# Performance work log

Hardware: AMD Instinct MI355X
Metric: run time of the kernel (lower is better)

The kernel has to match this reference:

```python
import jax, jax.numpy as jnp
import numpy as np

B, T, I, H, O = 128, 512, 512, 2048, 512  # batch, seq_length, input, hidden, output


def setup_inputs() -> dict:
    key = jax.random.key(0)
    ks = jax.random.split(key, 8)
    s_ih = 1.0 / np.sqrt(H)  # torch RNNCell/Linear default init scale 1/sqrt(hidden)
    body = jax.random.normal(ks[0], (B, T - 1, I), dtype=jnp.float32)
    # last timestep row stores the integer pad index (as float), per the module's protocol
    pad = jax.random.randint(ks[1], (B,), 0, T - 2)
    last = jnp.broadcast_to(pad[:, None, None].astype(jnp.float32), (B, 1, I))
    x = jnp.concatenate([body, last], axis=1)  # [B, T, I]
    W_ih = jax.random.uniform(ks[2], (H, I), jnp.float32, -s_ih, s_ih)
    W_hh = jax.random.uniform(ks[3], (H, H), jnp.float32, -s_ih, s_ih)
    b_ih = jax.random.uniform(ks[4], (H,), jnp.float32, -s_ih, s_ih)
    b_hh = jax.random.uniform(ks[5], (H,), jnp.float32, -s_ih, s_ih)
    W_fc = jax.random.uniform(ks[6], (O, H), jnp.float32, -s_ih, s_ih)
    b_fc = jax.random.uniform(ks[7], (O,), jnp.float32, -s_ih, s_ih)
    h0 = jnp.ones((H,), jnp.float32)  # self.h parameter, ones-initialized
    return {"x": x, "h0": h0, "W_ih": W_ih, "b_ih": b_ih, "W_hh": W_hh,
            "b_hh": b_hh, "W_fc": W_fc, "b_fc": b_fc}


def reference(x, h0, W_ih, b_ih, W_hh, b_hh, W_fc, b_fc):
    steps = T - 2  # loop runs over x.shape[2]-1 = (T-1)-1 timesteps
    pad = x[:, -1, 0].astype(jnp.int32)          # [B] pad indices
    xs = jnp.transpose(x[:, :steps, :], (1, 0, 2))  # [steps, B, I]
    h_init = jnp.broadcast_to(h0, (x.shape[0], H))  # self.h * ones([B,1])

    def step(h, xt):
        h = jnp.tanh(xt @ W_ih.T + b_ih + h @ W_hh.T + b_hh)
        return h, h @ W_fc.T + b_fc

    _, outs = jax.lax.scan(step, h_init, xs)     # [steps, B, O]
    # mask selects the single timestep j == pad_len[b]; everything else is zeroed
    mask = (pad[None, :] == jnp.arange(steps)[:, None]).astype(outs.dtype)  # [steps, B]
    return jnp.sum(outs * mask[:, :, None], axis=0)  # [B, O]
```

## Files before the change

kernel.cpp:

```cpp
#include <hip/hip_runtime.h>

#define Bsz 128
#define Tsz 512
#define Isz 512
#define Hsz 2048
#define Osz 512
#define STEPS 510

typedef short short8 __attribute__((ext_vector_type(8)));
typedef float floatx4 __attribute__((ext_vector_type(4)));

__device__ __forceinline__ unsigned short f2bf(float f) {
  unsigned int u = __builtin_bit_cast(unsigned int, f);
  u += 0x7FFFu + ((u >> 16) & 1u);
  return (unsigned short)(u >> 16);
}

__device__ __forceinline__ float tanh_fast(float x) {
  const float e = __expf(2.f * x);
  return 1.f - 2.f * __builtin_amdgcn_rcpf(e + 1.f);
}

template <int AUX>
__device__ __forceinline__ void gload_lds16(const void* g, void* l) {
  __builtin_amdgcn_global_load_lds(
      (const __attribute__((address_space(1))) void*)g,
      (__attribute__((address_space(3))) void*)l, 16, 0, AUX);
}

__global__ __launch_bounds__(256, 1)
void rnn_kernel(const float* __restrict__ x, const float* __restrict__ h0v,
                const float* __restrict__ W_ih, const float* __restrict__ b_ih,
                const float* __restrict__ W_hh, const float* __restrict__ b_hh,
                unsigned short* __restrict__ hbuf,
                float* __restrict__ hfinal,
                unsigned int* __restrict__ flags,
                unsigned int* __restrict__ xcc_arr)
{
  __shared__ short h_lds[4 * 8192];
  __shared__ float red_lds[4 * 1024];
  __shared__ int pad_lds[16];
  __shared__ unsigned int mode_lds;

  const int tid = threadIdx.x;
  const int lane = tid & 63;
  const int wv = tid >> 6;
  const int m16 = lane & 15;
  const int quad = lane >> 4;
  const int m7 = m16 & 7;
  const int rg = blockIdx.x & 7;
  const int cg = blockIdx.x >> 3;
  const int b0 = rg * 16;
  const int c0 = cg * 64;
  const int kq = wv * 512;
  const int kqx = wv * 128;
  const int wvoff = wv * 8192;

  {
    unsigned int xcc;
    asm volatile("s_getreg_b32 %0, hwreg(HW_REG_XCC_ID)" : "=s"(xcc));
    if (tid == 0)
      __hip_atomic_store(&xcc_arr[rg * 32 + cg], xcc + 1u, __ATOMIC_RELAXED,
                         __HIP_MEMORY_SCOPE_AGENT);
    if (wv == 0) {
      const unsigned int* ap = &xcc_arr[rg * 32 + (lane & 31)];
      unsigned int v;
      do {
        v = __hip_atomic_load(ap, __ATOMIC_RELAXED, __HIP_MEMORY_SCOPE_AGENT);
        if (__all((int)(v != 0u))) break;
        __builtin_amdgcn_s_sleep(2);
      } while (true);
      const int same = __all((int)(v == xcc + 1u));
      if (tid == 0) mode_lds = (unsigned int)same;
    }
  }

  short8 wf[16][4];
  short8 wih[4][4];
#pragma unroll
  for (int nt = 0; nt < 4; ++nt) {
    const int wrow = c0 + nt * 16 + m16;
    const float* base = W_hh + (size_t)wrow * Hsz + kq + quad * 8;
#pragma unroll
    for (int kc = 0; kc < 16; ++kc) {
      short8 v;
#pragma unroll
      for (int j = 0; j < 8; ++j) v[j] = (short)f2bf(base[kc * 32 + j]);
      wf[kc][nt] = v;
    }
    const float* basex = W_ih + (size_t)wrow * Isz + kqx + quad * 8;
#pragma unroll
    for (int kc = 0; kc < 4; ++kc) {
      short8 v;
#pragma unroll
      for (int j = 0; j < 8; ++j) v[j] = (short)f2bf(basex[kc * 32 + j]);
      wih[kc][nt] = v;
    }
  }

  const int rrow = tid >> 4;
  const int rcb = (tid & 15) * 4;
  float bias[4];
#pragma unroll
  for (int i = 0; i < 4; ++i) bias[i] = b_ih[c0 + rcb + i] + b_hh[c0 + rcb + i];

  if (tid < 16)
    pad_lds[tid] = (int)x[(size_t)(b0 + tid) * (Tsz * Isz) + (size_t)(Tsz - 1) * Isz];

  for (int i = lane; i < 1024; i += 64) {
    const int c = i >> 7;
    const int r = (i >> 3) & 15;
    const int u = i & 7;
    const int k = kq + c * 64 + u * 8;
    short8 v;
#pragma unroll
    for (int j = 0; j < 8; ++j) v[j] = (short)f2bf(h0v[k + j]);
    *reinterpret_cast<short8*>(&h_lds[wvoff + c * 1024 + r * 64 + (u ^ (r & 7)) * 8]) = v;
  }

  __syncthreads();
  const bool use_l2 = (mode_lds != 0u);

  const unsigned int* fp = flags + (size_t)(wv * 8 + (lane & 7)) * 8 + rg;

  for (int t = 0; t < STEPS; ++t) {
    const bool have_next = (t + 1) < STEPS;

    const float* xp = x + (size_t)(b0 + m16) * (Tsz * Isz) + (size_t)t * Isz + kqx + quad * 8;
    float4 xv[8];
#pragma unroll
    for (int kcc = 0; kcc < 4; ++kcc) {
      xv[2 * kcc] = *reinterpret_cast<const float4*>(xp + kcc * 32);
      xv[2 * kcc + 1] = *reinterpret_cast<const float4*>(xp + kcc * 32 + 4);
    }

    if (t > 0) {
      while (!__all((int)(__hip_atomic_load(fp, __ATOMIC_RELAXED,
                                            __HIP_MEMORY_SCOPE_AGENT) >= (unsigned)t)))
        __builtin_amdgcn_s_sleep(1);
      const unsigned short* hsrcp = hbuf + (size_t)(t & 1) * (Bsz * Hsz);
      if (use_l2) {
#pragma unroll
        for (int c = 0; c < 8; ++c) {
          const unsigned short* src = hsrcp + (size_t)((wv * 8 + c) * 8 + rg) * 1024;
          gload_lds16<0x01>(src + lane * 8, &h_lds[wvoff + c * 1024]);
          gload_lds16<0x01>(src + 512 + lane * 8, &h_lds[wvoff + c * 1024 + 512]);
        }
      } else {
#pragma unroll
        for (int c = 0; c < 8; ++c) {
          const unsigned short* src = hsrcp + (size_t)((wv * 8 + c) * 8 + rg) * 1024;
          gload_lds16<0x11>(src + lane * 8, &h_lds[wvoff + c * 1024]);
          gload_lds16<0x11>(src + 512 + lane * 8, &h_lds[wvoff + c * 1024 + 512]);
        }
      }
    }

    short8 xa[4];
#pragma unroll
    for (int kcc = 0; kcc < 4; ++kcc) {
      short8 a;
      a[0] = (short)f2bf(xv[2 * kcc].x);
      a[1] = (short)f2bf(xv[2 * kcc].y);
      a[2] = (short)f2bf(xv[2 * kcc].z);
      a[3] = (short)f2bf(xv[2 * kcc].w);
      a[4] = (short)f2bf(xv[2 * kcc + 1].x);
      a[5] = (short)f2bf(xv[2 * kcc + 1].y);
      a[6] = (short)f2bf(xv[2 * kcc + 1].z);
      a[7] = (short)f2bf(xv[2 * kcc + 1].w);
      xa[kcc] = a;
    }

    floatx4 acc[4];
#pragma unroll
    for (int nt = 0; nt < 4; ++nt) {
      floatx4 zero = {0.f, 0.f, 0.f, 0.f};
      acc[nt] = zero;
    }
#pragma unroll
    for (int kcc = 0; kcc < 4; ++kcc)
#pragma unroll
      for (int nt = 0; nt < 4; ++nt)
        acc[nt] = __builtin_amdgcn_mfma_f32_16x16x32_bf16(xa[kcc], wih[kcc][nt], acc[nt], 0, 0, 0);

    __builtin_amdgcn_s_waitcnt(0x0F78);
#pragma unroll
    for (int c = 0; c < 4; ++c) {
      const int base = wvoff + c * 1024 + m16 * 64;
#pragma unroll
      for (int k2 = 0; k2 < 2; ++k2) {
        const short8 a =
            *reinterpret_cast<const short8*>(&h_lds[base + ((k2 * 4 + quad) ^ m7) * 8]);
#pragma unroll
        for (int nt = 0; nt < 4; ++nt)
          acc[nt] = __builtin_amdgcn_mfma_f32_16x16x32_bf16(a, wf[c * 2 + k2][nt], acc[nt], 0, 0, 0);
      }
    }
    __builtin_amdgcn_s_waitcnt(0x0F70);
#pragma unroll
    for (int c = 4; c < 8; ++c) {
      const int base = wvoff + c * 1024 + m16 * 64;
#pragma unroll
      for (int k2 = 0; k2 < 2; ++k2) {
        const short8 a =
            *reinterpret_cast<const short8*>(&h_lds[base + ((k2 * 4 + quad) ^ m7) * 8]);
#pragma unroll
        for (int nt = 0; nt < 4; ++nt)
          acc[nt] = __builtin_amdgcn_mfma_f32_16x16x32_bf16(a, wf[c * 2 + k2][nt], acc[nt], 0, 0, 0);
      }
    }

#pragma unroll
    for (int nt = 0; nt < 4; ++nt)
#pragma unroll
      for (int i = 0; i < 4; ++i)
        red_lds[wv * 1024 + (quad * 4 + i) * 64 + nt * 16 + m16] = acc[nt][i];

    __syncthreads();

    {
      float4 z = {0.f, 0.f, 0.f, 0.f};
#pragma unroll
      for (int ww = 0; ww < 4; ++ww) {
        const float4 p =
            *reinterpret_cast<const float4*>(&red_lds[ww * 1024 + rrow * 64 + rcb]);
        z.x += p.x; z.y += p.y; z.z += p.z; z.w += p.w;
      }
      const float t0 = tanh_fast(z.x + bias[0]);
      const float t1 = tanh_fast(z.y + bias[1]);
      const float t2 = tanh_fast(z.z + bias[2]);
      const float t3 = tanh_fast(z.w + bias[3]);
      unsigned long long pk = (unsigned long long)f2bf(t0) |
                              ((unsigned long long)f2bf(t1) << 16) |
                              ((unsigned long long)f2bf(t2) << 32) |
                              ((unsigned long long)f2bf(t3) << 48);
      const int toff = rrow * 64 + ((rcb >> 3) ^ (rrow & 7)) * 8 + ((rcb >> 2) & 1) * 4;
      unsigned short* hd = hbuf + (size_t)((t + 1) & 1) * (Bsz * Hsz) +
                           (size_t)(cg * 8 + rg) * 1024 + toff;
      if (use_l2) {
        *reinterpret_cast<unsigned long long*>(hd) = pk;
      } else {
        __hip_atomic_store(reinterpret_cast<unsigned long long*>(hd), pk,
                           __ATOMIC_RELAXED, __HIP_MEMORY_SCOPE_AGENT);
      }
      if (pad_lds[rrow] == t) {
        float4 o;
        o.x = t0; o.y = t1; o.z = t2; o.w = t3;
        *reinterpret_cast<float4*>(&hfinal[(size_t)(b0 + rrow) * Hsz + c0 + rcb]) = o;
      }
    }

    __syncthreads();

    if (have_next && tid == 0) {
      __hip_atomic_store(flags + cg * 8 + rg, (unsigned)(t + 1),
                         __ATOMIC_RELAXED, __HIP_MEMORY_SCOPE_AGENT);
    }
  }
}

__global__ __launch_bounds__(64)
void fc_kernel(const float* __restrict__ hfinal, const float* __restrict__ W_fc,
               const float* __restrict__ b_fc, float* __restrict__ out) {
  const int lane = threadIdx.x & 63;
  const int m16 = lane & 15;
  const int quad = lane >> 4;
  const int b0 = (blockIdx.x & 7) * 16;
  const int o0 = (blockIdx.x >> 3) * 16;
  floatx4 acc = {0.f, 0.f, 0.f, 0.f};
  const float* ap = hfinal + (size_t)(b0 + m16) * Hsz + quad * 8;
  const float* bp = W_fc + (size_t)(o0 + m16) * Hsz + quad * 8;
#pragma unroll 4
  for (int kc = 0; kc < 64; ++kc) {
    short8 a, b;
#pragma unroll
    for (int j = 0; j < 8; ++j) a[j] = (short)f2bf(ap[kc * 32 + j]);
#pragma unroll
    for (int j = 0; j < 8; ++j) b[j] = (short)f2bf(bp[kc * 32 + j]);
    acc = __builtin_amdgcn_mfma_f32_16x16x32_bf16(a, b, acc, 0, 0, 0);
  }
  const float bias = b_fc[o0 + m16];
#pragma unroll
  for (int i = 0; i < 4; ++i)
    out[(size_t)(b0 + quad * 4 + i) * Osz + o0 + m16] = acc[i] + bias;
}

__global__ void zero_flags(unsigned int* f) { f[blockIdx.x * 256 + threadIdx.x] = 0u; }

extern "C" void kernel_launch(void* const* d_in, const int* in_sizes, int n_in,
                              void* d_out, int out_size, void* d_ws, size_t ws_size,
                              hipStream_t stream) {
  const float* x = (const float*)d_in[0];
  const float* h0 = (const float*)d_in[1];
  const float* W_ih = (const float*)d_in[2];
  const float* b_ih = (const float*)d_in[3];
  const float* W_hh = (const float*)d_in[4];
  const float* b_hh = (const float*)d_in[5];
  const float* W_fc = (const float*)d_in[6];
  const float* b_fc = (const float*)d_in[7];
  float* out = (float*)d_out;

  char* ws = (char*)d_ws;
  unsigned short* hbuf = (unsigned short*)ws;
  float* hfinal = (float*)(ws + (1u << 20));
  unsigned int* flags = (unsigned int*)(ws + (2u << 20));
  unsigned int* xcc_arr = flags + 256;

  zero_flags<<<2, 256, 0, stream>>>(flags);
  rnn_kernel<<<256, 256, 0, stream>>>(x, h0, W_ih, b_ih, W_hh, b_hh, hbuf, hfinal,
                                      flags, xcc_arr);
  fc_kernel<<<256, 64, 0, stream>>>(hfinal, W_fc, b_fc, out);
}
```

Measured before the change: 2.070 ms.

## Prefetch next timestep's x into double-buffered LDS via async global-to-LDS loads

Replaces the per-step direct global loads of the x slice with an asynchronous global_load_lds prefetch of the next timestep into a swizzled, double-buffered LDS area, issued right after the h exchange loads. The x fetch latency can then overlap with the cross-block flag wait and the MFMA work instead of sitting at the start of each step. The vmcnt waits are re-encoded so the h halves are consumed while the x prefetch stays in flight, and __syncthreads is replaced with a barrier that only waits on lgkmcnt. The cost is extra LDS use and correctness that relies on the atomic spin or the barrier draining the prefetch before the next step reads it.

```diff
diff --git a/kernel.cpp b/kernel.cpp
--- a/kernel.cpp
+++ b/kernel.cpp
@@ -26,6 +26,10 @@
   __builtin_amdgcn_global_load_lds(
       (const __attribute__((address_space(1))) void*)g,
       (__attribute__((address_space(3))) void*)l, 16, 0, AUX);
+}
+
+__device__ __forceinline__ void barrier_lds() {
+  asm volatile("s_waitcnt lgkmcnt(0)\n\ts_barrier" ::: "memory");
 }
 
 __global__ __launch_bounds__(256, 1)
@@ -38,6 +42,7 @@
                 unsigned int* __restrict__ xcc_arr)
 {
   __shared__ short h_lds[4 * 8192];
+  __shared__ float x_lds[2 * 4 * 2048];
   __shared__ float red_lds[4 * 1024];
   __shared__ int pad_lds[16];
   __shared__ unsigned int mode_lds;
@@ -118,6 +123,16 @@
     *reinterpret_cast<short8*>(&h_lds[wvoff + c * 1024 + r * 64 + (u ^ (r & 7)) * 8]) = v;
   }
 
+  {
+#pragma unroll
+    for (int c = 0; c < 8; ++c) {
+      const int r = 2 * c + (lane >> 5);
+      const float* g = x + (size_t)(b0 + r) * (Tsz * Isz) + kqx +
+                       (((lane & 31) ^ (r & 7)) << 2);
+      gload_lds16<0>(g, &x_lds[wv * 2048 + c * 256]);
+    }
+  }
+
   __syncthreads();
   const bool use_l2 = (mode_lds != 0u);
 
@@ -125,14 +140,7 @@
 
   for (int t = 0; t < STEPS; ++t) {
     const bool have_next = (t + 1) < STEPS;
-
-    const float* xp = x + (size_t)(b0 + m16) * (Tsz * Isz) + (size_t)t * Isz + kqx + quad * 8;
-    float4 xv[8];
-#pragma unroll
-    for (int kcc = 0; kcc < 4; ++kcc) {
-      xv[2 * kcc] = *reinterpret_cast<const float4*>(xp + kcc * 32);
-      xv[2 * kcc + 1] = *reinterpret_cast<const float4*>(xp + kcc * 32 + 4);
-    }
+    const int par = t & 1;
 
     if (t > 0) {
       while (!__all((int)(__hip_atomic_load(fp, __ATOMIC_RELAXED,
@@ -156,19 +164,32 @@
       }
     }
 
+    if (have_next) {
+      const int npar = par ^ 1;
+#pragma unroll
+      for (int c = 0; c < 8; ++c) {
+        const int r = 2 * c + (lane >> 5);
+        const float* g = x + (size_t)(b0 + r) * (Tsz * Isz) + (size_t)(t + 1) * Isz +
+                         kqx + (((lane & 31) ^ (r & 7)) << 2);
+        gload_lds16<0>(g, &x_lds[(npar * 4 + wv) * 2048 + c * 256]);
+      }
+    }
+
     short8 xa[4];
-#pragma unroll
-    for (int kcc = 0; kcc < 4; ++kcc) {
-      short8 a;
-      a[0] = (short)f2bf(xv[2 * kcc].x);
-      a[1] = (short)f2bf(xv[2 * kcc].y);
-      a[2] = (short)f2bf(xv[2 * kcc].z);
-      a[3] = (short)f2bf(xv[2 * kcc].w);
-      a[4] = (short)f2bf(xv[2 * kcc + 1].x);
-      a[5] = (short)f2bf(xv[2 * kcc + 1].y);
-      a[6] = (short)f2bf(xv[2 * kcc + 1].z);
-      a[7] = (short)f2bf(xv[2 * kcc + 1].w);
-      xa[kcc] = a;
+    {
+      const float* xb = &x_lds[(par * 4 + wv) * 2048 + m16 * 128];
+#pragma unroll
+      for (int kc = 0; kc < 4; ++kc) {
+        const int u0 = kc * 8 + quad * 2;
+        const float4 a0 = *reinterpret_cast<const float4*>(&xb[(u0 ^ m7) << 2]);
+        const float4 a1 = *reinterpret_cast<const float4*>(&xb[((u0 + 1) ^ m7) << 2]);
+        short8 a;
+        a[0] = (short)f2bf(a0.x); a[1] = (short)f2bf(a0.y);
+        a[2] = (short)f2bf(a0.z); a[3] = (short)f2bf(a0.w);
+        a[4] = (short)f2bf(a1.x); a[5] = (short)f2bf(a1.y);
+        a[6] = (short)f2bf(a1.z); a[7] = (short)f2bf(a1.w);
+        xa[kc] = a;
+      }
     }
 
     floatx4 acc[4];
@@ -183,7 +204,7 @@
       for (int nt = 0; nt < 4; ++nt)
         acc[nt] = __builtin_amdgcn_mfma_f32_16x16x32_bf16(xa[kcc], wih[kcc][nt], acc[nt], 0, 0, 0);
 
-    __builtin_amdgcn_s_waitcnt(0x0F78);
+    __builtin_amdgcn_s_waitcnt(0x4F70);
 #pragma unroll
     for (int c = 0; c < 4; ++c) {
       const int base = wvoff + c * 1024 + m16 * 64;
@@ -196,7 +217,7 @@
           acc[nt] = __builtin_amdgcn_mfma_f32_16x16x32_bf16(a, wf[c * 2 + k2][nt], acc[nt], 0, 0, 0);
       }
     }
-    __builtin_amdgcn_s_waitcnt(0x0F70);
+    __builtin_amdgcn_s_waitcnt(0x0F78);
 #pragma unroll
     for (int c = 4; c < 8; ++c) {
       const int base = wvoff + c * 1024 + m16 * 64;
@@ -216,7 +237,7 @@
       for (int i = 0; i < 4; ++i)
         red_lds[wv * 1024 + (quad * 4 + i) * 64 + nt * 16 + m16] = acc[nt][i];
 
-    __syncthreads();
+    barrier_lds();
 
     {
       float4 z = {0.f, 0.f, 0.f, 0.f};
```

New measurement: 3.140 ms. 1.52x slower.
